# Performance work log

Measured on AMD Instinct MI355X. Metric: run time of the kernel, lower is better.

The kernel has to match this reference:

```python
import jax, jax.numpy as jnp
import numpy as np

T, B, D = 2048, 16, 1024


def setup_inputs() -> dict:
    key = jax.random.key(0)
    ks = jax.random.split(key, 4)
    x = jax.random.normal(ks[0], (T, B, D), dtype=jnp.float32)
    z = jax.random.normal(ks[1], (T, B, D), dtype=jnp.float32)
    h0 = jnp.zeros((B, D), dtype=jnp.float32)
    # xavier-uniform-ish W_x, scaled near-orthogonal-ish W_h (random normal scaled)
    W_x = jax.random.normal(ks[2], (D, D), dtype=jnp.float32) * (1.0 / np.sqrt(D))
    W_h = jax.random.normal(ks[3], (D, D), dtype=jnp.float32) * (0.9 / np.sqrt(D))
    b = jnp.zeros((D,), dtype=jnp.float32)
    g_z = jnp.ones((D,), dtype=jnp.float32)
    g_h = jnp.zeros((D,), dtype=jnp.float32)
    b_gate = jnp.zeros((D,), dtype=jnp.float32)
    return {"x": x, "z": z, "h0": h0, "W_x": W_x, "W_h": W_h, "b": b,
            "g_z": g_z, "g_h": g_h, "b_gate": b_gate}


def reference(x, z, h0, W_x, W_h, b, g_z, g_h, b_gate):
    # Precompute the input projection for all timesteps in one big GEMM.
    xp = jnp.einsum('tbd,ed->tbe', x, W_x) + b  # [T,B,D]

    def step(h_prev, inp):
        xp_t, z_t = inp
        h_new = jnp.tanh(xp_t + h_prev @ W_h.T)           # [B,D]
        gate = jax.nn.silu(z_t * g_z + h_new * g_h + b_gate)
        out = h_new * gate
        return h_new, (out, h_new)

    _, (output, hs) = jax.lax.scan(step, h0, (xp, z))
    h = jnp.concatenate([h0[None], hs], axis=0)  # [T+1,B,D]
    return output, h
```

## Files before the change

### kernel.cpp

```cpp
#include <hip/hip_runtime.h>
#include <stdint.h>

#define T_STEPS 2048
#define BATCH   16
#define DIM     1024

typedef float    f32x4 __attribute__((ext_vector_type(4)));
typedef float    f32x2 __attribute__((ext_vector_type(2)));
typedef unsigned u32x4 __attribute__((ext_vector_type(4)));
typedef __bf16   bf16x8 __attribute__((ext_vector_type(8)));

__global__ void prep_kernel(const float* __restrict__ h0,
                            float* __restrict__ hout,
                            unsigned long long* __restrict__ hX) {
  int i = blockIdx.x * blockDim.x + threadIdx.x;
  if (i < BATCH * DIM) {
    float v = h0[i];
    hout[i] = v;
    hX[i] = (unsigned long long)__float_as_uint(v);
    hX[BATCH * DIM + i] = 0xFFFFFFFF00000000ull;
  }
}

__global__ __launch_bounds__(256)
void xp_gemm(const float* __restrict__ X, const float* __restrict__ W,
             const float* __restrict__ Bv, float* __restrict__ XP) {
  __shared__ __bf16 As[128 * 64];
  __shared__ __bf16 Bs[128 * 64];
  const int tid = threadIdx.x;
  const int bm = blockIdx.x & 255;
  const int bn = blockIdx.x >> 8;
  const int w = tid >> 6, l = tid & 63;
  const int wr = w >> 1, wc = w & 1;
  const int sr = tid >> 1, sh = tid & 1;

  const float* xrow = X + (size_t)(bm * 128 + sr) * DIM + sh * 32;
  const float* wrow = W + (size_t)(bn * 128 + sr) * DIM + sh * 32;
  char* AsB = (char*)As;
  char* BsB = (char*)Bs;
  const int swr  = sr * 128;
  const int swzs = (sr & 7) << 4;

  f32x4 acc[4][4];
  const f32x4 z4 = {0.f, 0.f, 0.f, 0.f};
#pragma unroll
  for (int i = 0; i < 4; ++i)
#pragma unroll
    for (int j = 0; j < 4; ++j) acc[i][j] = z4;

  for (int kt = 0; kt < 16; ++kt) {
#pragma unroll
    for (int j = 0; j < 8; ++j) {
      f32x4 a  = *(const f32x4*)(xrow + kt * 64 + 4 * j);
      f32x4 bv = *(const f32x4*)(wrow + kt * 64 + 4 * j);
      union { __bf16 h[4]; unsigned long long u; } pa, pb;
#pragma unroll
      for (int q = 0; q < 4; ++q) { pa.h[q] = (__bf16)a[q]; pb.h[q] = (__bf16)bv[q]; }
      int c2  = (sh * 32 + 4 * j) * 2;
      int off = swr + (c2 ^ swzs);
      *(unsigned long long*)(AsB + off) = pa.u;
      *(unsigned long long*)(BsB + off) = pb.u;
    }
    __syncthreads();
#pragma unroll
    for (int ks = 0; ks < 2; ++ks) {
      bf16x8 afr[4], bfr[4];
#pragma unroll
      for (int mi = 0; mi < 4; ++mi) {
        int row = wr * 64 + mi * 16 + (l & 15);
        int c2  = ks * 64 + (l >> 4) * 16;
        afr[mi] = *(const bf16x8*)(AsB + row * 128 + (c2 ^ ((row & 7) << 4)));
      }
#pragma unroll
      for (int ni = 0; ni < 4; ++ni) {
        int row = wc * 64 + ni * 16 + (l & 15);
        int c2  = ks * 64 + (l >> 4) * 16;
        bfr[ni] = *(const bf16x8*)(BsB + row * 128 + (c2 ^ ((row & 7) << 4)));
      }
#pragma unroll
      for (int mi = 0; mi < 4; ++mi)
#pragma unroll
        for (int ni = 0; ni < 4; ++ni)
          acc[mi][ni] = __builtin_amdgcn_mfma_f32_16x16x32_bf16(
              afr[mi], bfr[ni], acc[mi][ni], 0, 0, 0);
    }
    __syncthreads();
  }
  const int colb = bn * 128 + wc * 64 + (l & 15);
#pragma unroll
  for (int ni = 0; ni < 4; ++ni) {
    int col = colb + ni * 16;
    float bb = Bv[col];
#pragma unroll
    for (int mi = 0; mi < 4; ++mi) {
      int row = bm * 128 + wr * 64 + mi * 16 + ((l >> 4) << 2);
#pragma unroll
      for (int r = 0; r < 4; ++r)
        XP[(size_t)(row + r) * DIM + col] = acc[mi][ni][r] + bb;
    }
  }
}

__global__ __launch_bounds__(1024, 4)
void rnn_kernel(const float* __restrict__ Wh, const float* __restrict__ Z,
                const float* __restrict__ gz, const float* __restrict__ gh,
                const float* __restrict__ bg,
                float* __restrict__ out,
                float* __restrict__ hout,
                unsigned long long* __restrict__ hX) {
  __shared__ float hb[2][1024];
  const int tid = threadIdx.x;
  const int w   = tid >> 6;
  const int l   = tid & 63;
  const int b   = blockIdx.x >> 4;
  const int s   = blockIdx.x & 15;
  const int r0  = s * 64;
  const int myrow  = r0 + w * 4 + (l & 3);
  const bool writer = (l < 4);

  f32x4 W4[4][4];
  {
    const f32x4* WhV = (const f32x4*)Wh;
#pragma unroll
    for (int r4 = 0; r4 < 4; ++r4) {
      size_t base = (size_t)(r0 + w * 4 + r4) * (DIM / 4) + l * 4;
#pragma unroll
      for (int jj = 0; jj < 4; ++jj) W4[r4][jj] = WhV[base + jj];
    }
  }

  float cgz = 0.f, cgh = 0.f, cbg = 0.f, xp_n = 0.f, z_n = 0.f;
  if (writer) {
    cgz = gz[myrow]; cgh = gh[myrow]; cbg = bg[myrow];
    xp_n = out[(size_t)b * DIM + myrow];
    z_n  = Z[(size_t)b * DIM + myrow];
  }

  unsigned long long* hx0 = hX + (size_t)b * DIM;
  unsigned long long* hx1 = hX + (size_t)(BATCH + b) * DIM;

  for (int t = 0; t < T_STEPS; ++t) {
    unsigned long long* src = (t & 1) ? hx1 : hx0;
    unsigned long long* dst = (t & 1) ? hx0 : hx1;

    if (w == 0) {
      const char* a0 = (const char*)src + 16 * l;
      const char* a1 = a0 + 4096;
      const unsigned tt = (unsigned)t;
      u32x4 q0, q1, q2, q3, q4, q5, q6, q7;
      int spins = 0;
      for (;;) {
        asm volatile(
            "global_load_dwordx4 %[q0], %[a0], off sc1\n\t"
            "global_load_dwordx4 %[q1], %[a0], off offset:1024 sc1\n\t"
            "global_load_dwordx4 %[q2], %[a0], off offset:2048 sc1\n\t"
            "global_load_dwordx4 %[q3], %[a0], off offset:3072 sc1\n\t"
            "global_load_dwordx4 %[q4], %[a1], off sc1\n\t"
            "global_load_dwordx4 %[q5], %[a1], off offset:1024 sc1\n\t"
            "global_load_dwordx4 %[q6], %[a1], off offset:2048 sc1\n\t"
            "global_load_dwordx4 %[q7], %[a1], off offset:3072 sc1\n\t"
            "s_waitcnt vmcnt(0)"
            : [q0]"=v"(q0), [q1]"=v"(q1), [q2]"=v"(q2), [q3]"=v"(q3),
              [q4]"=v"(q4), [q5]"=v"(q5), [q6]"=v"(q6), [q7]"=v"(q7)
            : [a0]"v"(a0), [a1]"v"(a1)
            : "memory");
        int ok = (q0.y == tt) & (q0.w == tt) & (q1.y == tt) & (q1.w == tt) &
                 (q2.y == tt) & (q2.w == tt) & (q3.y == tt) & (q3.w == tt) &
                 (q4.y == tt) & (q4.w == tt) & (q5.y == tt) & (q5.w == tt) &
                 (q6.y == tt) & (q6.w == tt) & (q7.y == tt) & (q7.w == tt);
        if (__all(ok)) break;
        if (++spins >= (1 << 22)) break;
        __builtin_amdgcn_s_sleep(2);
      }
#define SCAT(J, Q) { int w0 = 2 * l + 128 * J; w0 ^= ((w0 >> 5) & 7) << 2; \
      f32x2 p; p.x = __uint_as_float(Q.x); p.y = __uint_as_float(Q.z);      \
      *(f32x2*)&hb[t & 1][w0] = p; }
      SCAT(0, q0) SCAT(1, q1) SCAT(2, q2) SCAT(3, q3)
      SCAT(4, q4) SCAT(5, q5) SCAT(6, q6) SCAT(7, q7)
#undef SCAT
    }
    __syncthreads();

    float acc0 = 0.f, acc1 = 0.f, acc2 = 0.f, acc3 = 0.f;
#pragma unroll
    for (int jj = 0; jj < 4; ++jj) {
      int word = ((l << 4) | (jj << 2)) ^ (((l >> 1) & 7) << 2);
      f32x4 h4 = *(const f32x4*)&hb[t & 1][word];
#pragma unroll
      for (int i = 0; i < 4; ++i) {
        acc0 = fmaf(W4[0][jj][i], h4[i], acc0);
        acc1 = fmaf(W4[1][jj][i], h4[i], acc1);
        acc2 = fmaf(W4[2][jj][i], h4[i], acc2);
        acc3 = fmaf(W4[3][jj][i], h4[i], acc3);
      }
    }
    float w01 = (l & 1) ? acc0 : acc1;
    float v01 = ((l & 1) ? acc1 : acc0) + __shfl_xor(w01, 1);
    float w23 = (l & 1) ? acc2 : acc3;
    float v23 = ((l & 1) ? acc3 : acc2) + __shfl_xor(w23, 1);
    float wv  = (l & 2) ? v01 : v23;
    float vv  = ((l & 2) ? v23 : v01) + __shfl_xor(wv, 2);
    vv += __shfl_xor(vv, 4);
    vv += __shfl_xor(vv, 8);
    vv += __shfl_xor(vv, 16);
    vv += __shfl_xor(vv, 32);

    if (writer) {
      float pre = vv + xp_n;
      float e2 = __expf(2.0f * pre);
      float hn = 1.0f - 2.0f / (e2 + 1.0f);
      unsigned long long pk = ((unsigned long long)(unsigned)(t + 1) << 32)
                            | (unsigned long long)__float_as_uint(hn);
      __hip_atomic_store(&dst[myrow], pk, __ATOMIC_RELAXED, __HIP_MEMORY_SCOPE_AGENT);
      hout[((size_t)(t + 1) * BATCH + b) * DIM + myrow] = hn;
      float y   = z_n * cgz + hn * cgh + cbg;
      float sig = 1.0f / (1.0f + __expf(-y));
      out[((size_t)t * BATCH + b) * DIM + myrow] = hn * (y * sig);
      if (t + 1 < T_STEPS) {
        xp_n = out[((size_t)(t + 1) * BATCH + b) * DIM + myrow];
        z_n  = Z[((size_t)(t + 1) * BATCH + b) * DIM + myrow];
      }
    }
  }
}

extern "C" void kernel_launch(void* const* d_in, const int* in_sizes, int n_in,
                              void* d_out, int out_size, void* d_ws, size_t ws_size,
                              hipStream_t stream) {
  const float* x    = (const float*)d_in[0];
  const float* z    = (const float*)d_in[1];
  const float* h0   = (const float*)d_in[2];
  const float* Wx   = (const float*)d_in[3];
  const float* Wh   = (const float*)d_in[4];
  const float* bias = (const float*)d_in[5];
  const float* gz   = (const float*)d_in[6];
  const float* gh   = (const float*)d_in[7];
  const float* bg   = (const float*)d_in[8];

  float* out  = (float*)d_out;
  float* hout = out + (size_t)T_STEPS * BATCH * DIM;
  unsigned long long* hX = (unsigned long long*)d_ws;

  prep_kernel<<<dim3(64), dim3(256), 0, stream>>>(h0, hout, hX);
  xp_gemm<<<dim3(2048), dim3(256), 0, stream>>>(x, Wx, bias, out);
  rnn_kernel<<<dim3(256), dim3(1024), 0, stream>>>(Wh, z, gz, gh, bg, out, hout, hX);
}
```

Baseline: 5.547 ms.

## Distribute h polling across waves with per-wave sentinel flags and local h reuse

Replaces the single-wave poll of the full 1024-element hidden state with a split scheme. Each of 15 waves first spins on a compact sentinel array and then loads only its 64-element slice of remote blocks' h. Each block writes its own new h values directly into the other LDS buffer instead of reading them back from global memory. Wave 0's slice appears to be skipped, since q equals s for w=0, so that slice comes from the local write. This spreads polling latency across waves and shrinks the critical-path load, but it adds an extra sentinel store per wave per step and removes the spin timeout.

```diff
diff --git a/kernel.cpp b/kernel.cpp
--- a/kernel.cpp
+++ b/kernel.cpp
@@ -4,21 +4,27 @@
 #define T_STEPS 2048
 #define BATCH   16
 #define DIM     1024
+#define BD      (BATCH * DIM)
+#define SENTN   4096
 
 typedef float    f32x4 __attribute__((ext_vector_type(4)));
-typedef float    f32x2 __attribute__((ext_vector_type(2)));
 typedef unsigned u32x4 __attribute__((ext_vector_type(4)));
 typedef __bf16   bf16x8 __attribute__((ext_vector_type(8)));
 
 __global__ void prep_kernel(const float* __restrict__ h0,
                             float* __restrict__ hout,
-                            unsigned long long* __restrict__ hX) {
+                            unsigned long long* __restrict__ hX,
+                            unsigned* __restrict__ sent) {
   int i = blockIdx.x * blockDim.x + threadIdx.x;
-  if (i < BATCH * DIM) {
+  if (i < BD) {
     float v = h0[i];
     hout[i] = v;
     hX[i] = (unsigned long long)__float_as_uint(v);
-    hX[BATCH * DIM + i] = 0xFFFFFFFF00000000ull;
+    hX[BD + i] = 0xFFFFFFFF00000000ull;
+  }
+  if (i < SENTN) {
+    sent[i] = 0u;
+    sent[SENTN + i] = 0xFFFFFFFFu;
   }
 }
 
@@ -55,7 +61,7 @@
       f32x4 bv = *(const f32x4*)(wrow + kt * 64 + 4 * j);
       union { __bf16 h[4]; unsigned long long u; } pa, pb;
 #pragma unroll
-      for (int q = 0; q < 4; ++q) { pa.h[q] = (__bf16)a[q]; pb.h[q] = (__bf16)bv[q]; }
+      for (int qq = 0; qq < 4; ++qq) { pa.h[qq] = (__bf16)a[qq]; pb.h[qq] = (__bf16)bv[qq]; }
       int c2  = (sh * 32 + 4 * j) * 2;
       int off = swr + (c2 ^ swzs);
       *(unsigned long long*)(AsB + off) = pa.u;
@@ -101,13 +107,19 @@
   }
 }
 
+__device__ __forceinline__ int swz_word(int c) {
+  int q = c >> 2;
+  return (c & 3) | (((q ^ (q >> 3)) & 255) << 2);
+}
+
 __global__ __launch_bounds__(1024, 4)
 void rnn_kernel(const float* __restrict__ Wh, const float* __restrict__ Z,
                 const float* __restrict__ gz, const float* __restrict__ gh,
-                const float* __restrict__ bg,
+                const float* __restrict__ bg, const float* __restrict__ h0,
                 float* __restrict__ out,
                 float* __restrict__ hout,
-                unsigned long long* __restrict__ hX) {
+                unsigned long long* __restrict__ hX,
+                unsigned* __restrict__ sent) {
   __shared__ float hb[2][1024];
   const int tid = threadIdx.x;
   const int w   = tid >> 6;
@@ -115,6 +127,7 @@
   const int b   = blockIdx.x >> 4;
   const int s   = blockIdx.x & 15;
   const int r0  = s * 64;
+  const int q   = (s + w) & 15;
   const int myrow  = r0 + w * 4 + (l & 3);
   const bool writer = (l < 4);
 
@@ -128,6 +141,8 @@
       for (int jj = 0; jj < 4; ++jj) W4[r4][jj] = WhV[base + jj];
     }
   }
+
+  if (w == 0) hb[0][swz_word(r0 + l)] = h0[(size_t)b * DIM + r0 + l];
 
   float cgz = 0.f, cgh = 0.f, cbg = 0.f, xp_n = 0.f, z_n = 0.f;
   if (writer) {
@@ -136,56 +151,40 @@
     z_n  = Z[(size_t)b * DIM + myrow];
   }
 
-  unsigned long long* hx0 = hX + (size_t)b * DIM;
-  unsigned long long* hx1 = hX + (size_t)(BATCH + b) * DIM;
-
   for (int t = 0; t < T_STEPS; ++t) {
-    unsigned long long* src = (t & 1) ? hx1 : hx0;
-    unsigned long long* dst = (t & 1) ? hx0 : hx1;
-
-    if (w == 0) {
-      const char* a0 = (const char*)src + 16 * l;
-      const char* a1 = a0 + 4096;
-      const unsigned tt = (unsigned)t;
-      u32x4 q0, q1, q2, q3, q4, q5, q6, q7;
-      int spins = 0;
+    const int p  = t & 1;
+    const int p1 = p ^ 1;
+    const unsigned tt = (unsigned)t;
+    const unsigned long long* src = hX + (size_t)p * BD + (size_t)b * DIM;
+    unsigned long long*       dst = hX + (size_t)p1 * BD + (size_t)b * DIM;
+
+    if (w != 0) {
+      const unsigned* sp = sent + p * SENTN + b * 256 + q * 16 + (l & 15);
+      unsigned sv;
       for (;;) {
-        asm volatile(
-            "global_load_dwordx4 %[q0], %[a0], off sc1\n\t"
-            "global_load_dwordx4 %[q1], %[a0], off offset:1024 sc1\n\t"
-            "global_load_dwordx4 %[q2], %[a0], off offset:2048 sc1\n\t"
-            "global_load_dwordx4 %[q3], %[a0], off offset:3072 sc1\n\t"
-            "global_load_dwordx4 %[q4], %[a1], off sc1\n\t"
-            "global_load_dwordx4 %[q5], %[a1], off offset:1024 sc1\n\t"
-            "global_load_dwordx4 %[q6], %[a1], off offset:2048 sc1\n\t"
-            "global_load_dwordx4 %[q7], %[a1], off offset:3072 sc1\n\t"
-            "s_waitcnt vmcnt(0)"
-            : [q0]"=v"(q0), [q1]"=v"(q1), [q2]"=v"(q2), [q3]"=v"(q3),
-              [q4]"=v"(q4), [q5]"=v"(q5), [q6]"=v"(q6), [q7]"=v"(q7)
-            : [a0]"v"(a0), [a1]"v"(a1)
-            : "memory");
-        int ok = (q0.y == tt) & (q0.w == tt) & (q1.y == tt) & (q1.w == tt) &
-                 (q2.y == tt) & (q2.w == tt) & (q3.y == tt) & (q3.w == tt) &
-                 (q4.y == tt) & (q4.w == tt) & (q5.y == tt) & (q5.w == tt) &
-                 (q6.y == tt) & (q6.w == tt) & (q7.y == tt) & (q7.w == tt);
-        if (__all(ok)) break;
-        if (++spins >= (1 << 22)) break;
-        __builtin_amdgcn_s_sleep(2);
-      }
-#define SCAT(J, Q) { int w0 = 2 * l + 128 * J; w0 ^= ((w0 >> 5) & 7) << 2; \
-      f32x2 p; p.x = __uint_as_float(Q.x); p.y = __uint_as_float(Q.z);      \
-      *(f32x2*)&hb[t & 1][w0] = p; }
-      SCAT(0, q0) SCAT(1, q1) SCAT(2, q2) SCAT(3, q3)
-      SCAT(4, q4) SCAT(5, q5) SCAT(6, q6) SCAT(7, q7)
-#undef SCAT
+        asm volatile("global_load_dword %0, %1, off sc1\n\ts_waitcnt vmcnt(0)"
+                     : "=v"(sv) : "v"(sp) : "memory");
+        if (__all(sv == tt)) break;
+        __builtin_amdgcn_s_sleep(1);
+      }
+      const unsigned long long* ap = src + q * 64 + l;
+      unsigned long long v;
+      for (;;) {
+        asm volatile("global_load_dwordx2 %0, %1, off sc1\n\ts_waitcnt vmcnt(0)"
+                     : "=v"(v) : "v"(ap) : "memory");
+        if (__all((unsigned)(v >> 32) == tt)) break;
+        __builtin_amdgcn_s_sleep(1);
+      }
+      hb[p][swz_word(q * 64 + l)] = __uint_as_float((unsigned)v);
     }
     __syncthreads();
 
     float acc0 = 0.f, acc1 = 0.f, acc2 = 0.f, acc3 = 0.f;
 #pragma unroll
     for (int jj = 0; jj < 4; ++jj) {
-      int word = ((l << 4) | (jj << 2)) ^ (((l >> 1) & 7) << 2);
-      f32x4 h4 = *(const f32x4*)&hb[t & 1][word];
+      int qr = 4 * l + jj;
+      int wb = ((qr ^ (qr >> 3)) & 255) << 2;
+      f32x4 h4 = *(const f32x4*)&hb[p][wb];
 #pragma unroll
       for (int i = 0; i < 4; ++i) {
         acc0 = fmaf(W4[0][jj][i], h4[i], acc0);
@@ -212,6 +211,7 @@
       unsigned long long pk = ((unsigned long long)(unsigned)(t + 1) << 32)
                             | (unsigned long long)__float_as_uint(hn);
       __hip_atomic_store(&dst[myrow], pk, __ATOMIC_RELAXED, __HIP_MEMORY_SCOPE_AGENT);
+      hb[p1][swz_word(myrow)] = hn;
       hout[((size_t)(t + 1) * BATCH + b) * DIM + myrow] = hn;
       float y   = z_n * cgz + hn * cgh + cbg;
       float sig = 1.0f / (1.0f + __expf(-y));
@@ -220,6 +220,10 @@
         xp_n = out[((size_t)(t + 1) * BATCH + b) * DIM + myrow];
         z_n  = Z[((size_t)(t + 1) * BATCH + b) * DIM + myrow];
       }
+    }
+    if (l == 0) {
+      __hip_atomic_store(&sent[p1 * SENTN + b * 256 + s * 16 + w],
+                         (unsigned)(t + 1), __ATOMIC_RELAXED, __HIP_MEMORY_SCOPE_AGENT);
     }
   }
 }
@@ -240,8 +244,9 @@
   float* out  = (float*)d_out;
   float* hout = out + (size_t)T_STEPS * BATCH * DIM;
   unsigned long long* hX = (unsigned long long*)d_ws;
-
-  prep_kernel<<<dim3(64), dim3(256), 0, stream>>>(h0, hout, hX);
+  unsigned* sent = (unsigned*)((char*)d_ws + 2ull * BD * 8ull);
+
+  prep_kernel<<<dim3(64), dim3(256), 0, stream>>>(h0, hout, hX, sent);
   xp_gemm<<<dim3(2048), dim3(256), 0, stream>>>(x, Wx, bias, out);
-  rnn_kernel<<<dim3(256), dim3(1024), 0, stream>>>(Wh, z, gz, gh, bg, out, hout, hX);
-}
+  rnn_kernel<<<dim3(256), dim3(1024), 0, stream>>>(Wh, z, gz, gh, bg, h0, out, hout, hX, sent);
+}
```

Result: slower. 8.177 ms (+47.4%).
